# Optimization experiments

Measured on AMD Instinct MI355X. Metric: run time of the kernel, lower is better.

The kernel has to match this reference:

```python
import jax, jax.numpy as jnp
import numpy as np

B, NUM_OBJECTS, NUM_ATTRS, T = 8, 128, 4, 12
MAX_CONCEPTS, EMBED_DIM, IDENTITY_DIM, ATTENTION_DIM, HIDDEN_DIM = 2048, 128, 64, 64, 256
OP_MODE, OP_INSERT, OP_TRANSFER = 0, 1, 2


def setup_inputs() -> dict:
    key = jax.random.key(0)
    ks = jax.random.split(key, 24)
    def rn(k, shape, s=0.05):
        return s * jax.random.normal(k, shape, dtype=jnp.float32)
    return {
        'scene': jax.random.randint(ks[0], (B, NUM_OBJECTS, NUM_ATTRS), 0, MAX_CONCEPTS - 1),
        'program_op': jax.random.randint(ks[1], (B, T), 0, 3),
        'program_arg': jax.random.randint(ks[2], (B, T), 0, MAX_CONCEPTS),
        'attr_emb_in': rn(ks[3], (MAX_CONCEPTS, EMBED_DIM)),
        'attr_emb_out': rn(ks[4], (MAX_CONCEPTS, EMBED_DIM)),
        'attr_emb_id': rn(ks[5], (MAX_CONCEPTS, IDENTITY_DIM)),
        'concept_emb_in': rn(ks[6], (MAX_CONCEPTS, EMBED_DIM)),
        'concept_emb_out': rn(ks[7], (MAX_CONCEPTS, EMBED_DIM)),
        'concept_emb_id': rn(ks[8], (MAX_CONCEPTS, IDENTITY_DIM)),
        'embed_init': rn(ks[9], (EMBED_DIM,)),
        'identity_init': rn(ks[10], (IDENTITY_DIM,)),
        'attention_init': jnp.zeros((ATTENTION_DIM,), dtype=jnp.float32),
        'axon_w1': rn(ks[11], (HIDDEN_DIM, ATTENTION_DIM + IDENTITY_DIM)),
        'axon_b1': rn(ks[12], (HIDDEN_DIM,)),
        'axon_w2': rn(ks[13], (ATTENTION_DIM, HIDDEN_DIM)),
        'axon_b2': rn(ks[14], (ATTENTION_DIM,)),
        'meta_w1': rn(ks[15], (HIDDEN_DIM, EMBED_DIM + ATTENTION_DIM)),
        'meta_b1': rn(ks[16], (HIDDEN_DIM,)),
        'meta_w2': rn(ks[17], (ATTENTION_DIM, HIDDEN_DIM)),
        'meta_b2': rn(ks[18], (ATTENTION_DIM,)),
    }


def _mlp(x, w1, b1, w2, b2):
    # torch Linear convention: y = x @ W.T + b
    return jnp.maximum(x @ w1.T + b1, 0.0) @ w2.T + b2


def reference(scene, program_op, program_arg, attr_emb_in, attr_emb_out, attr_emb_id,
              concept_emb_in, concept_emb_out, concept_emb_id,
              embed_init, identity_init, attention_init,
              axon_w1, axon_b1, axon_w2, axon_b2,
              meta_w1, meta_b1, meta_w2, meta_b2):
    Bq, N, _ = scene.shape
    C = MAX_CONCEPTS + N  # dim_concept
    mask = (scene != -1).astype(jnp.float32)  # (B,N,A) non-background mask
    def embed_bg(E):
        return (E[scene + 1] * mask[..., None]).sum(2)  # (B,N,D)
    objects_in = embed_bg(attr_emb_in)
    objects_out = embed_bg(attr_emb_out)
    objects_id = embed_bg(attr_emb_id)

    rep = lambda w: jnp.broadcast_to(w[None], (Bq,) + w.shape)
    dendron = jnp.concatenate([rep(concept_emb_in), objects_in], 1)    # (B,C,E)
    axon = jnp.concatenate([rep(concept_emb_out), objects_out], 1)     # (B,C,E)
    identity = jnp.concatenate([rep(concept_emb_id), objects_id], 1)   # (B,C,Id)
    weight_matrix = jnp.einsum('bie,bje->bij', dendron, axon)           # (B,C,C)

    arguments = concept_emb_out[program_arg]                            # (B,T,E)
    is_mode = (program_op == OP_MODE).astype(jnp.float32)               # (B,T)
    is_insert = (program_op == OP_INSERT).astype(jnp.float32)
    is_transfer = (program_op == OP_TRANSFER).astype(jnp.float32)

    meta0 = jnp.broadcast_to(attention_init[None], (Bq, ATTENTION_DIM))
    att0 = jnp.broadcast_to(attention_init[None, None], (Bq, C, ATTENTION_DIM))

    def step(carry, xs):
        meta, attention = carry
        arg_i, m, ins, tr = xs  # (B,E), (B,), (B,), (B,)
        new_meta = _mlp(jnp.concatenate([meta, arg_i], 1), meta_w1, meta_b1, meta_w2, meta_b2)
        meta = m[:, None] * new_meta + (1.0 - m[:, None]) * meta
        # (arguments * axon).mean over embed dim -> (B,C)
        proj = jnp.einsum('be,bce->bc', arg_i, axon) / EMBED_DIM
        attention_insert = meta[:, None, :] * proj[:, :, None]          # (B,C,A)
        attended_weight = weight_matrix * attention.mean(2)[:, None, :] # (B,C,C)
        ia = jnp.concatenate([identity, attention], 2)                  # (B,C,Id+A)
        # (attended_weight[:,:,:,None] * ia[:,None]).mean(2) == matmul / C
        gathered = jnp.einsum('bij,bjd->bid', attended_weight, ia) / C  # (B,C,Id+A)
        attention_transfer = _mlp(gathered, axon_w1, axon_b1, axon_w2, axon_b2) + gathered[..., IDENTITY_DIM:]
        attention = attention + ins[:, None, None] * attention_insert + tr[:, None, None] * attention_transfer
        attention = jnp.clip(jnp.where(attention >= 0, attention, 0.01 * attention), -1.0, 2.0)
        return (meta, attention), (attention, attention_insert, attention_transfer)

    xs = (jnp.swapaxes(arguments, 0, 1), is_mode.T, is_insert.T, is_transfer.T)
    (meta, attention), (att_hist, ins_hist, trans_hist) = jax.lax.scan(step, (meta0, att0), xs)
    output_softmax = jax.nn.log_softmax(attention.mean(2), axis=1)  # (B,C)
    return (output_softmax, att_hist, ins_hist, trans_hist)
```

## Files before the change

kernel.cpp:

```cpp
#include <hip/hip_runtime.h>

#define B 8
#define NOBJ 128
#define NATTR 4
#define T 12
#define MC 2048
#define E 128
#define IDD 64
#define AD 64
#define HD 256
#define C 2176

typedef short s16x8 __attribute__((ext_vector_type(8)));
typedef float f32x4 __attribute__((ext_vector_type(4)));

__device__ inline unsigned short f2b(float f) {
  union { float f; unsigned u; } v; v.f = f;
  unsigned r = v.u + 0x7FFFu + ((v.u >> 16) & 1u);
  return (unsigned short)(r >> 16);
}
__device__ inline float b2f(unsigned short u) {
  union { unsigned u; float f; } v; v.u = ((unsigned)u) << 16;
  return v.f;
}

__device__ __forceinline__ void st_coh_u64(unsigned long long* p, unsigned long long v) {
  __hip_atomic_store(p, v, __ATOMIC_RELAXED, __HIP_MEMORY_SCOPE_AGENT);
}
__device__ __forceinline__ unsigned long long ld_coh_u64(const unsigned long long* p) {
  return __hip_atomic_load(p, __ATOMIC_RELAXED, __HIP_MEMORY_SCOPE_AGENT);
}
__device__ __forceinline__ void st_coh_u32(unsigned* p, unsigned v) {
  __hip_atomic_store(p, v, __ATOMIC_RELAXED, __HIP_MEMORY_SCOPE_AGENT);
}
__device__ __forceinline__ unsigned ld_coh_u32(const unsigned* p) {
  return __hip_atomic_load(p, __ATOMIC_RELAXED, __HIP_MEMORY_SCOPE_AGENT);
}

__device__ __forceinline__ int gidx(int r, int c) {
  return r * 128 + ((((c >> 3) ^ (r & 15)) << 3) | (c & 7));
}
__device__ __forceinline__ int hidx(int r, int c) {
  return r * 256 + ((((c >> 3) ^ (r & 15)) << 3) | (c & 7));
}
__device__ __forceinline__ int mtidx(int r, int c) {
  return r * 128 + ((((c >> 3) ^ (r & 15)) << 3) | (c & 7));
}

__global__ __launch_bounds__(256) void k_setup1(
    const int* __restrict__ scene,
    const float* __restrict__ aein, const float* __restrict__ aeout,
    const float* __restrict__ aeid,
    const float* __restrict__ cein, const float* __restrict__ ceout,
    const float* __restrict__ ceid,
    const float* __restrict__ aw1, const float* __restrict__ aw2,
    const float* __restrict__ mw1, const float* __restrict__ mw2,
    unsigned short* __restrict__ dendron_bf, float* __restrict__ axon,
    float* __restrict__ identity,
    unsigned short* __restrict__ w1_bf, unsigned short* __restrict__ w2_bf,
    float* __restrict__ mw1T, float* __restrict__ mw2T,
    unsigned* __restrict__ mflag) {
  int blk = blockIdx.x;
  int tid = threadIdx.x;
  if (blk < 4352) {
    int gid = blk * 2 + (tid >> 7);
    int e = tid & 127;
    int b = gid / C, j = gid % C;
    float din, dout, did = 0.f;
    if (j < MC) {
      din  = cein[j * E + e];
      dout = ceout[j * E + e];
      if (e < IDD) did = ceid[j * IDD + e];
    } else {
      int obj = j - MC;
      float sIn = 0.f, sOut = 0.f, sId = 0.f;
      for (int a = 0; a < NATTR; a++) {
        int s = scene[(b * NOBJ + obj) * NATTR + a];
        float m = (s != -1) ? 1.f : 0.f;
        int idx = s + 1;
        sIn  += aein[idx * E + e] * m;
        sOut += aeout[idx * E + e] * m;
        if (e < IDD) sId += aeid[idx * IDD + e] * m;
      }
      din = sIn; dout = sOut; did = sId;
    }
    dendron_bf[(size_t)gid * E + e] = f2b(din);
    axon[(size_t)gid * E + e] = dout;
    if (e < IDD) identity[(size_t)gid * IDD + e] = did;
  } else if (blk < 4544) {
    int i = (blk - 4352) * 256 + tid;
    if (i < HD * E)  w1_bf[i] = f2b(aw1[i]);
    if (i < AD * HD) w2_bf[i] = f2b(aw2[i]);
    if (i < 192 * HD) { int c = i / HD, k = i % HD; mw1T[c * HD + k] = mw1[k * 192 + c]; }
    if (i < HD * AD)  { int k = i / AD, a = i % AD; mw2T[k * AD + a] = mw2[a * HD + k]; }
  } else {
    if (tid < B * 16) mflag[tid] = 0u;
  }
}

__global__ __launch_bounds__(256) void k_setup2(
    const float* __restrict__ axon, const float* __restrict__ identity,
    const float* __restrict__ att_init,
    const int* __restrict__ prog_op, const int* __restrict__ prog_arg,
    const float* __restrict__ ceout,
    const float* __restrict__ mw1T, const float* __restrict__ mb1,
    const float* __restrict__ mw2T, const float* __restrict__ mb2,
    unsigned short* __restrict__ axonT, unsigned short* __restrict__ idT_g,
    unsigned short* __restrict__ siaT, float* __restrict__ att_g,
    float* __restrict__ meta_all, float* __restrict__ proj_all) {
  int blk = blockIdx.x;
  int tid = threadIdx.x;
  if (blk < 272) {
    int b = blk / 34, jc = blk % 34;
    int j0 = jc * 64;
    __shared__ float ax[64][129];
    __shared__ float idb[64][65];
    int lane = tid & 63, lr = lane & 15;
    float s = att_init[lane];
    s += __shfl_xor(s, 1, 64);  s += __shfl_xor(s, 2, 64);
    s += __shfl_xor(s, 4, 64);  s += __shfl_xor(s, 8, 64);
    s += __shfl_xor(s, 16, 64); s += __shfl_xor(s, 32, 64);
    float am0 = s * (1.f / AD);
    for (int i = tid; i < 64 * 128; i += 256) {
      int j = i >> 7, e = i & 127;
      ax[j][e] = axon[(size_t)(b * C + j0 + j) * E + e];
    }
    for (int i = tid; i < 64 * 64; i += 256) {
      int j = i >> 6, d = i & 63;
      idb[j][d] = identity[(size_t)(b * C + j0 + j) * IDD + d];
    }
    __syncthreads();
    for (int i = tid; i < 128 * 64; i += 256) {
      int e = i >> 6, jj = i & 63;
      axonT[(size_t)(b * E + e) * C + j0 + jj] = f2b(ax[jj][e]);
    }
    for (int i = tid; i < 64 * 64; i += 256) {
      int d = i >> 6, jj = i & 63;
      idT_g[(size_t)(b * 64 + d) * C + j0 + jj] = f2b(idb[jj][d]);
      siaT[(size_t)(b * 128 + d) * C + j0 + jj] = f2b(idb[jj][d] * am0);
      siaT[(size_t)(b * 128 + 64 + d) * C + j0 + jj] = f2b(att_init[d] * am0);
    }
    {
      float* ag = att_g + (size_t)blk * 4096 + tid * 16;
      #pragma unroll
      for (int n = 0; n < 4; n++) {
        float v0 = att_init[n * 16 + lr];
        #pragma unroll
        for (int v = 0; v < 4; v++) ag[n * 4 + v] = v0;
      }
    }
  } else if (blk < 280) {
    int b = blk - 272;
    __shared__ float x[192];
    __shared__ float h[HD];
    __shared__ float meta[AD];
    if (tid < AD) meta[tid] = att_init[tid];
    __syncthreads();
    for (int t = 0; t < T; t++) {
      int arg = prog_arg[b * T + t];
      if (tid < AD) x[tid] = meta[tid];
      else if (tid < 192) x[tid] = ceout[arg * E + (tid - 64)];
      __syncthreads();
      float s = mb1[tid];
      for (int c = 0; c < 192; c++) s += x[c] * mw1T[c * HD + tid];
      h[tid] = fmaxf(s, 0.f);
      __syncthreads();
      if (tid < AD) {
        float o = mb2[tid];
        for (int k = 0; k < HD; k++) o += h[k] * mw2T[k * AD + tid];
        float m = (prog_op[b * T + t] == 0) ? 1.f : 0.f;
        float nm = m * o + (1.f - m) * meta[tid];
        meta[tid] = nm;
        meta_all[(t * B + b) * AD + tid] = nm;
      }
      __syncthreads();
    }
  } else {
    int gid = (blk - 280) * 4 + (tid >> 6);
    int lane = tid & 63;
    int b = gid / C, i = gid % C;
    float a0 = axon[(size_t)gid * E + lane];
    float a1 = axon[(size_t)gid * E + 64 + lane];
    for (int t = 0; t < T; t++) {
      int arg = prog_arg[b * T + t];
      float p = a0 * ceout[arg * E + lane] + a1 * ceout[arg * E + 64 + lane];
      for (int off = 1; off < 64; off <<= 1) p += __shfl_xor(p, off, 64);
      if (lane == 0) proj_all[(size_t)(t * B + b) * C + i] = p * (1.f / E);
    }
  }
}

__global__ __launch_bounds__(256) void k_step(
    int t,
    const unsigned short* __restrict__ dendron_bf,
    const unsigned short* __restrict__ axonT,
    const unsigned short* __restrict__ idT_g,
    const unsigned short* __restrict__ siaT_in,
    const unsigned short* __restrict__ w1_bf, const float* __restrict__ b1g,
    const unsigned short* __restrict__ w2_bf, const float* __restrict__ b2g,
    const float* __restrict__ proj_all, const float* __restrict__ meta_all,
    const int* __restrict__ prog_op,
    unsigned long long* __restrict__ Mt64,
    float* __restrict__ att_g, unsigned short* __restrict__ siaT_out,
    float* __restrict__ rowmean,
    float* __restrict__ att_hist, float* __restrict__ ins_hist,
    float* __restrict__ trans_hist,
    unsigned* __restrict__ mflag) {
  const int blk = blockIdx.x;
  const int b = blk / 34, ch = blk % 34, j0 = ch * 64;
  const int tid = threadIdx.x;
  const int w = tid >> 6, lane = tid & 63, lr = lane & 15, lg = lane >> 4;

  __shared__ unsigned short smem[24576];
  __shared__ float am_l[64];
  unsigned short* g_l = smem;
  unsigned short* mt  = smem + 8192;
  unsigned short* h_l = smem + 8192;
  float* mred = (float*)smem;

  const f32x4 z = {0.f, 0.f, 0.f, 0.f};
  const unsigned ph = (unsigned)(t + 1);

  float att[4][4];
  {
    const f32x4* ag = (const f32x4*)(att_g + (size_t)blk * 4096 + tid * 16);
    #pragma unroll
    for (int n = 0; n < 4; n++) {
      f32x4 v4 = ag[n];
      #pragma unroll
      for (int v = 0; v < 4; v++) att[n][v] = v4[v];
    }
  }

  if (ch < 16) {
    int d0 = (ch >> 2) * 32, e0 = (ch & 3) * 32;
    const unsigned short* ap0 = siaT_in + (size_t)(b * 128 + d0 + lr) * C + w * 544 + lg * 8;
    const unsigned short* ap1 = ap0 + (size_t)16 * C;
    const unsigned short* bp0 = axonT + (size_t)(b * E + e0 + lr) * C + w * 544 + lg * 8;
    const unsigned short* bp1 = bp0 + (size_t)16 * C;
    f32x4 a00 = z, a01 = z, a10 = z, a11 = z;
    #pragma unroll 4
    for (int kk = 0; kk < 17; kk++) {
      int k0 = kk * 32;
      s16x8 A0 = *(const s16x8*)(ap0 + k0);
      s16x8 A1 = *(const s16x8*)(ap1 + k0);
      s16x8 B0 = *(const s16x8*)(bp0 + k0);
      s16x8 B1 = *(const s16x8*)(bp1 + k0);
      a00 = __builtin_amdgcn_mfma_f32_16x16x32_bf16(A0, B0, a00, 0, 0, 0);
      a01 = __builtin_amdgcn_mfma_f32_16x16x32_bf16(A0, B1, a01, 0, 0, 0);
      a10 = __builtin_amdgcn_mfma_f32_16x16x32_bf16(A1, B0, a10, 0, 0, 0);
      a11 = __builtin_amdgcn_mfma_f32_16x16x32_bf16(A1, B1, a11, 0, 0, 0);
    }
    #pragma unroll
    for (int v = 0; v < 4; v++) {
      mred[(w * 32 + lg * 4 + v) * 33 + lr]          = a00[v];
      mred[(w * 32 + lg * 4 + v) * 33 + 16 + lr]     = a01[v];
      mred[(w * 32 + 16 + lg * 4 + v) * 33 + lr]     = a10[v];
      mred[(w * 32 + 16 + lg * 4 + v) * 33 + 16 + lr] = a11[v];
    }
    __syncthreads();
    {
      int r = tid >> 3, c = (tid & 7) * 4;
      float s0 = 0.f, s1 = 0.f, s2 = 0.f, s3 = 0.f;
      #pragma unroll
      for (int w4 = 0; w4 < 4; w4++) {
        const float* p = &mred[(w4 * 32 + r) * 33 + c];
        s0 += p[0]; s1 += p[1]; s2 += p[2]; s3 += p[3];
      }
      unsigned long long pk = (unsigned long long)f2b(s0)
                            | ((unsigned long long)f2b(s1) << 16)
                            | ((unsigned long long)f2b(s2) << 32)
                            | ((unsigned long long)f2b(s3) << 48);
      st_coh_u64(Mt64 + (((size_t)(b * 128 + d0 + r) * 128) + e0 + c) / 4, pk);
    }
    asm volatile("s_waitcnt vmcnt(0)" ::: "memory");
    __syncthreads();
    if (tid == 0) st_coh_u32(mflag + b * 16 + ch, ph);
  }
  if (tid < 16) {
    while (ld_coh_u32(mflag + b * 16 + tid) < ph) __builtin_amdgcn_s_sleep(1);
  }
  __syncthreads();
  {
    const unsigned long long* mtp = Mt64 + (size_t)b * 4096;
    #pragma unroll
    for (int k = 0; k < 16; k++) {
      int idx = tid + k * 256;
      unsigned long long v = ld_coh_u64(mtp + idx);
      int r = idx >> 5, c4 = (idx & 31) * 4;
      *(unsigned long long*)&mt[mtidx(r, c4)] = v;
    }
  }
  __syncthreads();
  {
    s16x8 afr[4];
    #pragma unroll
    for (int ke = 0; ke < 4; ke++)
      afr[ke] = *(const s16x8*)(dendron_bf + (size_t)(b * C + j0 + w * 16 + lr) * E + ke * 32 + lg * 8);
    #pragma unroll
    for (int n = 0; n < 8; n++) {
      f32x4 acc = z;
      #pragma unroll
      for (int ke = 0; ke < 4; ke++) {
        s16x8 bf = *(const s16x8*)&mt[mtidx(n * 16 + lr, ke * 32 + lg * 8)];
        acc = __builtin_amdgcn_mfma_f32_16x16x32_bf16(afr[ke], bf, acc, 0, 0, 0);
      }
      #pragma unroll
      for (int v = 0; v < 4; v++)
        g_l[gidx(w * 16 + lg * 4 + v, n * 16 + lr)] = f2b(acc[v] * (1.f / C));
    }
  }
  __syncthreads();
  {
    s16x8 gf[4];
    #pragma unroll
    for (int kd = 0; kd < 4; kd++)
      gf[kd] = *(const s16x8*)&g_l[gidx(w * 16 + lr, kd * 32 + lg * 8)];
    #pragma unroll
    for (int n = 0; n < 16; n++) {
      f32x4 acc = z;
      #pragma unroll
      for (int kd = 0; kd < 4; kd++) {
        s16x8 bf = *(const s16x8*)(w1_bf + (size_t)(n * 16 + lr) * E + kd * 32 + lg * 8);
        acc = __builtin_amdgcn_mfma_f32_16x16x32_bf16(gf[kd], bf, acc, 0, 0, 0);
      }
      float b1v = b1g[n * 16 + lr];
      #pragma unroll
      for (int v = 0; v < 4; v++)
        h_l[hidx(w * 16 + lg * 4 + v, n * 16 + lr)] = f2b(fmaxf(acc[v] + b1v, 0.f));
    }
  }
  __syncthreads();
  {
    s16x8 hf[8];
    #pragma unroll
    for (int kk = 0; kk < 8; kk++)
      hf[kk] = *(const s16x8*)&h_l[hidx(w * 16 + lr, kk * 32 + lg * 8)];
    int op = prog_op[b * T + t];
    float insF = (op == 1) ? 1.f : 0.f, trF = (op == 2) ? 1.f : 0.f;
    float projv[4];
    #pragma unroll
    for (int v = 0; v < 4; v++)
      projv[v] = proj_all[(size_t)(t * B + b) * C + j0 + w * 16 + lg * 4 + v];
    #pragma unroll
    for (int n = 0; n < 4; n++) {
      f32x4 acc = z;
      #pragma unroll
      for (int kk = 0; kk < 8; kk++) {
        s16x8 bf = *(const s16x8*)(w2_bf + (size_t)(n * 16 + lr) * HD + kk * 32 + lg * 8);
        acc = __builtin_amdgcn_mfma_f32_16x16x32_bf16(hf[kk], bf, acc, 0, 0, 0);
      }
      int a = n * 16 + lr;
      float b2v = b2g[a];
      float meta_a = meta_all[(size_t)(t * B + b) * AD + a];
      #pragma unroll
      for (int v = 0; v < 4; v++) {
        int row = lg * 4 + v;
        int i = j0 + w * 16 + row;
        float transfer = acc[v] + b2v + b2f(g_l[gidx(w * 16 + row, 64 + a)]);
        float insert = meta_a * projv[v];
        float attv = att[n][v] + insF * insert + trF * transfer;
        attv = (attv >= 0.f) ? attv : 0.01f * attv;
        attv = fminf(fmaxf(attv, -1.f), 2.f);
        att[n][v] = attv;
        size_t hi = (((size_t)t * B + b) * C + i) * AD + a;
        __builtin_nontemporal_store(attv, att_hist + hi);
        __builtin_nontemporal_store(insert, ins_hist + hi);
        __builtin_nontemporal_store(transfer, trans_hist + hi);
      }
    }
  }
  float amr[4];
  {
    float s[4];
    #pragma unroll
    for (int v = 0; v < 4; v++) s[v] = att[0][v] + att[1][v] + att[2][v] + att[3][v];
    #pragma unroll
    for (int v = 0; v < 4; v++) {
      s[v] += __shfl_xor(s[v], 1, 64);
      s[v] += __shfl_xor(s[v], 2, 64);
      s[v] += __shfl_xor(s[v], 4, 64);
      s[v] += __shfl_xor(s[v], 8, 64);
      amr[v] = s[v] * (1.f / AD);
    }
    if (lr == 0) {
      #pragma unroll
      for (int v = 0; v < 4; v++) {
        am_l[w * 16 + lg * 4 + v] = amr[v];
        rowmean[(size_t)b * C + j0 + w * 16 + lg * 4 + v] = amr[v];
      }
    }
  }
  {
    f32x4* ag = (f32x4*)(att_g + (size_t)blk * 4096 + tid * 16);
    #pragma unroll
    for (int n = 0; n < 4; n++) {
      f32x4 v4;
      #pragma unroll
      for (int v = 0; v < 4; v++) v4[v] = att[n][v];
      ag[n] = v4;
      unsigned long long pk = 0;
      #pragma unroll
      for (int v = 0; v < 4; v++)
        pk |= (unsigned long long)f2b(att[n][v] * amr[v]) << (16 * v);
      *(unsigned long long*)(siaT_out + (size_t)(b * 128 + 64 + n * 16 + lr) * C + j0 + w * 16 + lg * 4) = pk;
    }
  }
  __syncthreads();
  #pragma unroll
  for (int k = 0; k < 2; k++) {
    int idx = tid + k * 256;
    int d = idx >> 3, part = idx & 7;
    int j = part * 8;
    s16x8 iv = *(const s16x8*)(idT_g + (size_t)(b * 64 + d) * C + j0 + j);
    s16x8 ov;
    #pragma unroll
    for (int m = 0; m < 8; m++)
      ov[m] = (short)f2b(b2f((unsigned short)iv[m]) * am_l[j + m]);
    *(s16x8*)(siaT_out + (size_t)(b * 128 + d) * C + j0 + j) = ov;
  }
}

__global__ void k_softmax(const float* __restrict__ rowmean, float* __restrict__ out) {
  int b = blockIdx.x;
  __shared__ float am[C];
  __shared__ float red[256];
  int tid = threadIdx.x;
  for (int i = tid; i < C; i += 256) am[i] = rowmean[(size_t)b * C + i];
  __syncthreads();
  float mx = -1e30f;
  for (int i = tid; i < C; i += 256) mx = fmaxf(mx, am[i]);
  red[tid] = mx; __syncthreads();
  for (int s = 128; s > 0; s >>= 1) { if (tid < s) red[tid] = fmaxf(red[tid], red[tid + s]); __syncthreads(); }
  mx = red[0]; __syncthreads();
  float sm = 0.f;
  for (int i = tid; i < C; i += 256) sm += expf(am[i] - mx);
  red[tid] = sm; __syncthreads();
  for (int s = 128; s > 0; s >>= 1) { if (tid < s) red[tid] += red[tid + s]; __syncthreads(); }
  float lse = logf(red[0]) + mx;
  for (int i = tid; i < C; i += 256) out[(size_t)b * C + i] = am[i] - lse;
}

extern "C" void kernel_launch(void* const* d_in, const int* in_sizes, int n_in,
                              void* d_out, int out_size, void* d_ws, size_t ws_size,
                              hipStream_t stream) {
  const int* scene     = (const int*)d_in[0];
  const int* prog_op   = (const int*)d_in[1];
  const int* prog_arg  = (const int*)d_in[2];
  const float* aein    = (const float*)d_in[3];
  const float* aeout   = (const float*)d_in[4];
  const float* aeid    = (const float*)d_in[5];
  const float* cein    = (const float*)d_in[6];
  const float* ceout   = (const float*)d_in[7];
  const float* ceid    = (const float*)d_in[8];
  const float* att_init = (const float*)d_in[11];
  const float* aw1 = (const float*)d_in[12];
  const float* ab1 = (const float*)d_in[13];
  const float* aw2 = (const float*)d_in[14];
  const float* ab2 = (const float*)d_in[15];
  const float* mw1 = (const float*)d_in[16];
  const float* mb1 = (const float*)d_in[17];
  const float* mw2 = (const float*)d_in[18];
  const float* mb2 = (const float*)d_in[19];

  char* ws = (char*)d_ws;
  size_t off = 0;
  auto carve = [&](size_t bytes) { char* p = ws + off; off += (bytes + 255) & ~(size_t)255; return p; };
  float* axon      = (float*)carve((size_t)B * C * E * 4);
  float* identity  = (float*)carve((size_t)B * C * IDD * 4);
  float* proj_all  = (float*)carve((size_t)T * B * C * 4);
  float* meta_all  = (float*)carve((size_t)T * B * AD * 4);
  float* mw1T      = (float*)carve((size_t)192 * HD * 4);
  float* mw2T      = (float*)carve((size_t)HD * AD * 4);
  float* rowmean   = (float*)carve((size_t)B * C * 4);
  float* att_g     = (float*)carve((size_t)272 * 4096 * 4);
  unsigned short* dendron_bf = (unsigned short*)carve((size_t)B * C * E * 2);
  unsigned short* axonT      = (unsigned short*)carve((size_t)B * E * C * 2);
  unsigned short* idT_g      = (unsigned short*)carve((size_t)B * 64 * C * 2);
  unsigned short* siaT       = (unsigned short*)carve((size_t)B * 128 * C * 2);
  unsigned long long* Mt64   = (unsigned long long*)carve((size_t)B * 4096 * 8);
  unsigned short* w1_bf      = (unsigned short*)carve((size_t)HD * E * 2);
  unsigned short* w2_bf      = (unsigned short*)carve((size_t)AD * HD * 2);
  unsigned*       mflag      = (unsigned*)carve(1024);

  float* out_sm     = (float*)d_out;
  float* att_hist   = out_sm + B * C;
  float* ins_hist   = att_hist + (size_t)T * B * C * AD;
  float* trans_hist = ins_hist + (size_t)T * B * C * AD;

  k_setup1<<<dim3(4545), dim3(256), 0, stream>>>(scene, aein, aeout, aeid, cein, ceout, ceid,
                                                 aw1, aw2, mw1, mw2,
                                                 dendron_bf, axon, identity,
                                                 w1_bf, w2_bf, mw1T, mw2T, mflag);
  k_setup2<<<dim3(1368), dim3(256), 0, stream>>>(axon, identity, att_init,
                                                 prog_op, prog_arg, ceout,
                                                 mw1T, mb1, mw2T, mb2,
                                                 axonT, idT_g, siaT, att_g,
                                                 meta_all, proj_all);
  for (int t = 0; t < T; t++) {
    k_step<<<dim3(272), dim3(256), 0, stream>>>(t, dendron_bf, axonT, idT_g, siaT,
                                                w1_bf, ab1, w2_bf, ab2,
                                                proj_all, meta_all, prog_op,
                                                Mt64, att_g, siaT, rowmean,
                                                att_hist, ins_hist, trans_hist, mflag);
  }
  k_softmax<<<dim3(B), dim3(256), 0, stream>>>(rowmean, out_sm);
}
```

Before: 655.4 us.

## Fuse all timesteps and softmax into one persistent kernel with flag-based sync

```diff
diff --git a/kernel.cpp b/kernel.cpp
--- a/kernel.cpp
+++ b/kernel.cpp
@@ -35,6 +35,21 @@
 }
 __device__ __forceinline__ unsigned ld_coh_u32(const unsigned* p) {
   return __hip_atomic_load(p, __ATOMIC_RELAXED, __HIP_MEMORY_SCOPE_AGENT);
+}
+__device__ __forceinline__ void st_coh_f32(float* p, float v) {
+  union { float f; unsigned u; } c; c.f = v;
+  __hip_atomic_store((unsigned*)p, c.u, __ATOMIC_RELAXED, __HIP_MEMORY_SCOPE_AGENT);
+}
+__device__ __forceinline__ float ld_coh_f32(const float* p) {
+  union { unsigned u; float f; } c;
+  c.u = __hip_atomic_load((const unsigned*)p, __ATOMIC_RELAXED, __HIP_MEMORY_SCOPE_AGENT);
+  return c.f;
+}
+__device__ __forceinline__ s16x8 ld_coh_b16x8(const unsigned short* p) {
+  union { unsigned long long u[2]; s16x8 v; } r;
+  r.u[0] = ld_coh_u64((const unsigned long long*)p);
+  r.u[1] = ld_coh_u64((const unsigned long long*)p + 1);
+  return r.v;
 }
 
 __device__ __forceinline__ int gidx(int r, int c) {
@@ -59,7 +74,7 @@
     float* __restrict__ identity,
     unsigned short* __restrict__ w1_bf, unsigned short* __restrict__ w2_bf,
     float* __restrict__ mw1T, float* __restrict__ mw2T,
-    unsigned* __restrict__ mflag) {
+    unsigned* __restrict__ flags) {
   int blk = blockIdx.x;
   int tid = threadIdx.x;
   if (blk < 4352) {
@@ -94,7 +109,7 @@
     if (i < 192 * HD) { int c = i / HD, k = i % HD; mw1T[c * HD + k] = mw1[k * 192 + c]; }
     if (i < HD * AD)  { int k = i / AD, a = i % AD; mw2T[k * AD + a] = mw2[a * HD + k]; }
   } else {
-    if (tid < B * 16) mflag[tid] = 0u;
+    for (int i = tid; i < 576; i += 256) flags[i] = 0u;
   }
 }
 
@@ -106,7 +121,7 @@
     const float* __restrict__ mw1T, const float* __restrict__ mb1,
     const float* __restrict__ mw2T, const float* __restrict__ mb2,
     unsigned short* __restrict__ axonT, unsigned short* __restrict__ idT_g,
-    unsigned short* __restrict__ siaT, float* __restrict__ att_g,
+    unsigned short* __restrict__ siaT,
     float* __restrict__ meta_all, float* __restrict__ proj_all) {
   int blk = blockIdx.x;
   int tid = threadIdx.x;
@@ -115,7 +130,7 @@
     int j0 = jc * 64;
     __shared__ float ax[64][129];
     __shared__ float idb[64][65];
-    int lane = tid & 63, lr = lane & 15;
+    int lane = tid & 63;
     float s = att_init[lane];
     s += __shfl_xor(s, 1, 64);  s += __shfl_xor(s, 2, 64);
     s += __shfl_xor(s, 4, 64);  s += __shfl_xor(s, 8, 64);
@@ -139,15 +154,6 @@
       idT_g[(size_t)(b * 64 + d) * C + j0 + jj] = f2b(idb[jj][d]);
       siaT[(size_t)(b * 128 + d) * C + j0 + jj] = f2b(idb[jj][d] * am0);
       siaT[(size_t)(b * 128 + 64 + d) * C + j0 + jj] = f2b(att_init[d] * am0);
-    }
-    {
-      float* ag = att_g + (size_t)blk * 4096 + tid * 16;
-      #pragma unroll
-      for (int n = 0; n < 4; n++) {
-        float v0 = att_init[n * 16 + lr];
-        #pragma unroll
-        for (int v = 0; v < 4; v++) ag[n * 4 + v] = v0;
-      }
     }
   } else if (blk < 280) {
     int b = blk - 272;
@@ -190,22 +196,21 @@
   }
 }
 
-__global__ __launch_bounds__(256) void k_step(
-    int t,
+__global__ __launch_bounds__(256, 2) void k_steps(
     const unsigned short* __restrict__ dendron_bf,
     const unsigned short* __restrict__ axonT,
     const unsigned short* __restrict__ idT_g,
-    const unsigned short* __restrict__ siaT_in,
+    unsigned short* __restrict__ siaT,
     const unsigned short* __restrict__ w1_bf, const float* __restrict__ b1g,
     const unsigned short* __restrict__ w2_bf, const float* __restrict__ b2g,
     const float* __restrict__ proj_all, const float* __restrict__ meta_all,
-    const int* __restrict__ prog_op,
+    const int* __restrict__ prog_op, const float* __restrict__ att_init,
     unsigned long long* __restrict__ Mt64,
-    float* __restrict__ att_g, unsigned short* __restrict__ siaT_out,
-    float* __restrict__ rowmean,
+    float* __restrict__ rowmean, float* __restrict__ out,
     float* __restrict__ att_hist, float* __restrict__ ins_hist,
     float* __restrict__ trans_hist,
-    unsigned* __restrict__ mflag) {
+    unsigned* __restrict__ mflag, unsigned* __restrict__ cflag,
+    unsigned* __restrict__ sflag) {
   const int blk = blockIdx.x;
   const int b = blk / 34, ch = blk % 34, j0 = ch * 64;
   const int tid = threadIdx.x;
@@ -213,232 +218,250 @@
 
   __shared__ unsigned short smem[24576];
   __shared__ float am_l[64];
+  __shared__ float red[256];
   unsigned short* g_l = smem;
   unsigned short* mt  = smem + 8192;
   unsigned short* h_l = smem + 8192;
-  float* mred = (float*)smem;
 
   const f32x4 z = {0.f, 0.f, 0.f, 0.f};
-  const unsigned ph = (unsigned)(t + 1);
 
   float att[4][4];
-  {
-    const f32x4* ag = (const f32x4*)(att_g + (size_t)blk * 4096 + tid * 16);
+  #pragma unroll
+  for (int n = 0; n < 4; n++) {
+    float v0 = att_init[n * 16 + lr];
     #pragma unroll
-    for (int n = 0; n < 4; n++) {
-      f32x4 v4 = ag[n];
-      #pragma unroll
-      for (int v = 0; v < 4; v++) att[n][v] = v4[v];
-    }
+    for (int v = 0; v < 4; v++) att[n][v] = v0;
   }
-
-  if (ch < 16) {
-    int d0 = (ch >> 2) * 32, e0 = (ch & 3) * 32;
-    const unsigned short* ap0 = siaT_in + (size_t)(b * 128 + d0 + lr) * C + w * 544 + lg * 8;
-    const unsigned short* ap1 = ap0 + (size_t)16 * C;
-    const unsigned short* bp0 = axonT + (size_t)(b * E + e0 + lr) * C + w * 544 + lg * 8;
-    const unsigned short* bp1 = bp0 + (size_t)16 * C;
-    f32x4 a00 = z, a01 = z, a10 = z, a11 = z;
-    #pragma unroll 4
-    for (int kk = 0; kk < 17; kk++) {
-      int k0 = kk * 32;
-      s16x8 A0 = *(const s16x8*)(ap0 + k0);
-      s16x8 A1 = *(const s16x8*)(ap1 + k0);
-      s16x8 B0 = *(const s16x8*)(bp0 + k0);
-      s16x8 B1 = *(const s16x8*)(bp1 + k0);
-      a00 = __builtin_amdgcn_mfma_f32_16x16x32_bf16(A0, B0, a00, 0, 0, 0);
-      a01 = __builtin_amdgcn_mfma_f32_16x16x32_bf16(A0, B1, a01, 0, 0, 0);
-      a10 = __builtin_amdgcn_mfma_f32_16x16x32_bf16(A1, B0, a10, 0, 0, 0);
-      a11 = __builtin_amdgcn_mfma_f32_16x16x32_bf16(A1, B1, a11, 0, 0, 0);
-    }
-    #pragma unroll
-    for (int v = 0; v < 4; v++) {
-      mred[(w * 32 + lg * 4 + v) * 33 + lr]          = a00[v];
-      mred[(w * 32 + lg * 4 + v) * 33 + 16 + lr]     = a01[v];
-      mred[(w * 32 + 16 + lg * 4 + v) * 33 + lr]     = a10[v];
-      mred[(w * 32 + 16 + lg * 4 + v) * 33 + 16 + lr] = a11[v];
+  s16x8 afr[4];
+  #pragma unroll
+  for (int ke = 0; ke < 4; ke++)
+    afr[ke] = *(const s16x8*)(dendron_bf + (size_t)(b * C + j0 + w * 16 + lr) * E + ke * 32 + lg * 8);
+
+  float amr[4];
+
+  for (int t = 0; t < T; t++) {
+    const unsigned ph = (unsigned)(t + 1);
+    if (ch < 4) {
+      if (t > 0) {
+        if (tid < 34) {
+          while (ld_coh_u32(cflag + b * 34 + tid) < (unsigned)t) __builtin_amdgcn_s_sleep(2);
+        }
+      }
+      __syncthreads();
+      const int d0 = ch * 32;
+      const int eh = w & 1, kh = w >> 1;
+      const int kbase = kh * 1088;
+      const unsigned short* ap0 = siaT + (size_t)(b * 128 + d0 + lr) * C + kbase + lg * 8;
+      const unsigned short* ap1 = ap0 + (size_t)16 * C;
+      const unsigned short* bp  = axonT + (size_t)(b * E + eh * 64 + lr) * C + kbase + lg * 8;
+      f32x4 pa[2][4];
+      #pragma unroll
+      for (int dp = 0; dp < 2; dp++)
+        #pragma unroll
+        for (int n = 0; n < 4; n++) pa[dp][n] = z;
+      for (int kk = 0; kk < 34; kk++) {
+        int k0 = kk * 32;
+        s16x8 A0 = ld_coh_b16x8(ap0 + k0);
+        s16x8 A1 = ld_coh_b16x8(ap1 + k0);
+        #pragma unroll
+        for (int n = 0; n < 4; n++) {
+          s16x8 Bn = *(const s16x8*)(bp + (size_t)n * 16 * C + k0);
+          pa[0][n] = __builtin_amdgcn_mfma_f32_16x16x32_bf16(A0, Bn, pa[0][n], 0, 0, 0);
+          pa[1][n] = __builtin_amdgcn_mfma_f32_16x16x32_bf16(A1, Bn, pa[1][n], 0, 0, 0);
+        }
+      }
+      float* pls = (float*)smem;
+      #pragma unroll
+      for (int dp = 0; dp < 2; dp++)
+        #pragma unroll
+        for (int n = 0; n < 4; n++)
+          #pragma unroll
+          for (int v = 0; v < 4; v++)
+            pls[(kh * 32 + dp * 16 + lg * 4 + v) * 132 + eh * 64 + n * 16 + lr] = pa[dp][n][v];
+      __syncthreads();
+      {
+        int r = tid >> 3, cb = (tid & 7) * 16;
+        const float* p0 = pls + r * 132 + cb;
+        const float* p1 = pls + (32 + r) * 132 + cb;
+        #pragma unroll
+        for (int q = 0; q < 4; q++) {
+          unsigned long long pk = 0;
+          #pragma unroll
+          for (int x = 0; x < 4; x++) {
+            float sv = p0[q * 4 + x] + p1[q * 4 + x];
+            pk |= (unsigned long long)f2b(sv) << (16 * x);
+          }
+          st_coh_u64(Mt64 + ((size_t)(b * 128 + d0 + r) * 128 + cb + q * 4) / 4, pk);
+        }
+      }
+      asm volatile("s_waitcnt vmcnt(0)" ::: "memory");
+      __syncthreads();
+      if (tid == 0) st_coh_u32(mflag + b * 4 + ch, ph);
+    }
+    if (tid < 4) {
+      while (ld_coh_u32(mflag + b * 4 + tid) < ph) __builtin_amdgcn_s_sleep(2);
     }
     __syncthreads();
     {
-      int r = tid >> 3, c = (tid & 7) * 4;
-      float s0 = 0.f, s1 = 0.f, s2 = 0.f, s3 = 0.f;
-      #pragma unroll
-      for (int w4 = 0; w4 < 4; w4++) {
-        const float* p = &mred[(w4 * 32 + r) * 33 + c];
-        s0 += p[0]; s1 += p[1]; s2 += p[2]; s3 += p[3];
-      }
-      unsigned long long pk = (unsigned long long)f2b(s0)
-                            | ((unsigned long long)f2b(s1) << 16)
-                            | ((unsigned long long)f2b(s2) << 32)
-                            | ((unsigned long long)f2b(s3) << 48);
-      st_coh_u64(Mt64 + (((size_t)(b * 128 + d0 + r) * 128) + e0 + c) / 4, pk);
-    }
-    asm volatile("s_waitcnt vmcnt(0)" ::: "memory");
-    __syncthreads();
-    if (tid == 0) st_coh_u32(mflag + b * 16 + ch, ph);
+      const unsigned long long* mtp = Mt64 + (size_t)b * 4096;
+      #pragma unroll
+      for (int k = 0; k < 16; k++) {
+        int idx = tid + k * 256;
+        unsigned long long v = ld_coh_u64(mtp + idx);
+        int r = idx >> 5, c4 = (idx & 31) * 4;
+        *(unsigned long long*)&mt[mtidx(r, c4)] = v;
+      }
+    }
+    __syncthreads();
+    {
+      #pragma unroll
+      for (int n = 0; n < 8; n++) {
+        f32x4 acc = z;
+        #pragma unroll
+        for (int ke = 0; ke < 4; ke++) {
+          s16x8 bf = *(const s16x8*)&mt[mtidx(n * 16 + lr, ke * 32 + lg * 8)];
+          acc = __builtin_amdgcn_mfma_f32_16x16x32_bf16(afr[ke], bf, acc, 0, 0, 0);
+        }
+        #pragma unroll
+        for (int v = 0; v < 4; v++)
+          g_l[gidx(w * 16 + lg * 4 + v, n * 16 + lr)] = f2b(acc[v] * (1.f / C));
+      }
+    }
+    __syncthreads();
+    {
+      s16x8 gf[4];
+      #pragma unroll
+      for (int kd = 0; kd < 4; kd++)
+        gf[kd] = *(const s16x8*)&g_l[gidx(w * 16 + lr, kd * 32 + lg * 8)];
+      #pragma unroll
+      for (int n = 0; n < 16; n++) {
+        f32x4 acc = z;
+        #pragma unroll
+        for (int kd = 0; kd < 4; kd++) {
+          s16x8 bf = *(const s16x8*)(w1_bf + (size_t)(n * 16 + lr) * E + kd * 32 + lg * 8);
+          acc = __builtin_amdgcn_mfma_f32_16x16x32_bf16(gf[kd], bf, acc, 0, 0, 0);
+        }
+        float b1v = b1g[n * 16 + lr];
+        #pragma unroll
+        for (int v = 0; v < 4; v++)
+          h_l[hidx(w * 16 + lg * 4 + v, n * 16 + lr)] = f2b(fmaxf(acc[v] + b1v, 0.f));
+      }
+    }
+    __syncthreads();
+    {
+      s16x8 hf[8];
+      #pragma unroll
+      for (int kk = 0; kk < 8; kk++)
+        hf[kk] = *(const s16x8*)&h_l[hidx(w * 16 + lr, kk * 32 + lg * 8)];
+      int op = prog_op[b * T + t];
+      float insF = (op == 1) ? 1.f : 0.f, trF = (op == 2) ? 1.f : 0.f;
+      float projv[4];
+      #pragma unroll
+      for (int v = 0; v < 4; v++)
+        projv[v] = proj_all[(size_t)(t * B + b) * C + j0 + w * 16 + lg * 4 + v];
+      #pragma unroll
+      for (int n = 0; n < 4; n++) {
+        f32x4 acc = z;
+        #pragma unroll
+        for (int kk = 0; kk < 8; kk++) {
+          s16x8 bf = *(const s16x8*)(w2_bf + (size_t)(n * 16 + lr) * HD + kk * 32 + lg * 8);
+          acc = __builtin_amdgcn_mfma_f32_16x16x32_bf16(hf[kk], bf, acc, 0, 0, 0);
+        }
+        int a = n * 16 + lr;
+        float b2v = b2g[a];
+        float meta_a = meta_all[(size_t)(t * B + b) * AD + a];
+        #pragma unroll
+        for (int v = 0; v < 4; v++) {
+          int row = lg * 4 + v;
+          int i = j0 + w * 16 + row;
+          float transfer = acc[v] + b2v + b2f(g_l[gidx(w * 16 + row, 64 + a)]);
+          float insert = meta_a * projv[v];
+          float attv = att[n][v] + insF * insert + trF * transfer;
+          attv = (attv >= 0.f) ? attv : 0.01f * attv;
+          attv = fminf(fmaxf(attv, -1.f), 2.f);
+          att[n][v] = attv;
+          size_t hi = (((size_t)t * B + b) * C + i) * AD + a;
+          __builtin_nontemporal_store(attv, att_hist + hi);
+          __builtin_nontemporal_store(insert, ins_hist + hi);
+          __builtin_nontemporal_store(transfer, trans_hist + hi);
+        }
+      }
+    }
+    {
+      float s[4];
+      #pragma unroll
+      for (int v = 0; v < 4; v++) s[v] = att[0][v] + att[1][v] + att[2][v] + att[3][v];
+      #pragma unroll
+      for (int v = 0; v < 4; v++) {
+        s[v] += __shfl_xor(s[v], 1, 64);
+        s[v] += __shfl_xor(s[v], 2, 64);
+        s[v] += __shfl_xor(s[v], 4, 64);
+        s[v] += __shfl_xor(s[v], 8, 64);
+        amr[v] = s[v] * (1.f / AD);
+      }
+      if (lr == 0) {
+        #pragma unroll
+        for (int v = 0; v < 4; v++) am_l[w * 16 + lg * 4 + v] = amr[v];
+      }
+    }
+    if (t < T - 1) {
+      #pragma unroll
+      for (int n = 0; n < 4; n++) {
+        unsigned long long pk = 0;
+        #pragma unroll
+        for (int v = 0; v < 4; v++)
+          pk |= (unsigned long long)f2b(att[n][v] * amr[v]) << (16 * v);
+        st_coh_u64((unsigned long long*)(siaT + (size_t)(b * 128 + 64 + n * 16 + lr) * C + j0 + w * 16 + lg * 4), pk);
+      }
+      __syncthreads();
+      #pragma unroll
+      for (int k2 = 0; k2 < 2; k2++) {
+        int idx = tid + k2 * 256;
+        int d = idx >> 3, part = idx & 7;
+        int j = part * 8;
+        s16x8 iv = *(const s16x8*)(idT_g + (size_t)(b * 64 + d) * C + j0 + j);
+        union { s16x8 v; unsigned long long u[2]; } ov;
+        #pragma unroll
+        for (int m = 0; m < 8; m++)
+          ov.v[m] = (short)f2b(b2f((unsigned short)iv[m]) * am_l[j + m]);
+        unsigned long long* dst = (unsigned long long*)(siaT + (size_t)(b * 128 + d) * C + j0 + j);
+        st_coh_u64(dst, ov.u[0]);
+        st_coh_u64(dst + 1, ov.u[1]);
+      }
+      asm volatile("s_waitcnt vmcnt(0)" ::: "memory");
+      __syncthreads();
+      if (tid == 0) st_coh_u32(cflag + b * 34 + ch, ph);
+      __syncthreads();
+    }
   }
-  if (tid < 16) {
-    while (ld_coh_u32(mflag + b * 16 + tid) < ph) __builtin_amdgcn_s_sleep(1);
-  }
-  __syncthreads();
-  {
-    const unsigned long long* mtp = Mt64 + (size_t)b * 4096;
-    #pragma unroll
-    for (int k = 0; k < 16; k++) {
-      int idx = tid + k * 256;
-      unsigned long long v = ld_coh_u64(mtp + idx);
-      int r = idx >> 5, c4 = (idx & 31) * 4;
-      *(unsigned long long*)&mt[mtidx(r, c4)] = v;
-    }
-  }
-  __syncthreads();
-  {
-    s16x8 afr[4];
-    #pragma unroll
-    for (int ke = 0; ke < 4; ke++)
-      afr[ke] = *(const s16x8*)(dendron_bf + (size_t)(b * C + j0 + w * 16 + lr) * E + ke * 32 + lg * 8);
-    #pragma unroll
-    for (int n = 0; n < 8; n++) {
-      f32x4 acc = z;
-      #pragma unroll
-      for (int ke = 0; ke < 4; ke++) {
-        s16x8 bf = *(const s16x8*)&mt[mtidx(n * 16 + lr, ke * 32 + lg * 8)];
-        acc = __builtin_amdgcn_mfma_f32_16x16x32_bf16(afr[ke], bf, acc, 0, 0, 0);
-      }
-      #pragma unroll
-      for (int v = 0; v < 4; v++)
-        g_l[gidx(w * 16 + lg * 4 + v, n * 16 + lr)] = f2b(acc[v] * (1.f / C));
-    }
-  }
-  __syncthreads();
-  {
-    s16x8 gf[4];
-    #pragma unroll
-    for (int kd = 0; kd < 4; kd++)
-      gf[kd] = *(const s16x8*)&g_l[gidx(w * 16 + lr, kd * 32 + lg * 8)];
-    #pragma unroll
-    for (int n = 0; n < 16; n++) {
-      f32x4 acc = z;
-      #pragma unroll
-      for (int kd = 0; kd < 4; kd++) {
-        s16x8 bf = *(const s16x8*)(w1_bf + (size_t)(n * 16 + lr) * E + kd * 32 + lg * 8);
-        acc = __builtin_amdgcn_mfma_f32_16x16x32_bf16(gf[kd], bf, acc, 0, 0, 0);
-      }
-      float b1v = b1g[n * 16 + lr];
-      #pragma unroll
-      for (int v = 0; v < 4; v++)
-        h_l[hidx(w * 16 + lg * 4 + v, n * 16 + lr)] = f2b(fmaxf(acc[v] + b1v, 0.f));
-    }
-  }
-  __syncthreads();
-  {
-    s16x8 hf[8];
-    #pragma unroll
-    for (int kk = 0; kk < 8; kk++)
-      hf[kk] = *(const s16x8*)&h_l[hidx(w * 16 + lr, kk * 32 + lg * 8)];
-    int op = prog_op[b * T + t];
-    float insF = (op == 1) ? 1.f : 0.f, trF = (op == 2) ? 1.f : 0.f;
-    float projv[4];
+  if (lr == 0) {
     #pragma unroll
     for (int v = 0; v < 4; v++)
-      projv[v] = proj_all[(size_t)(t * B + b) * C + j0 + w * 16 + lg * 4 + v];
-    #pragma unroll
-    for (int n = 0; n < 4; n++) {
-      f32x4 acc = z;
-      #pragma unroll
-      for (int kk = 0; kk < 8; kk++) {
-        s16x8 bf = *(const s16x8*)(w2_bf + (size_t)(n * 16 + lr) * HD + kk * 32 + lg * 8);
-        acc = __builtin_amdgcn_mfma_f32_16x16x32_bf16(hf[kk], bf, acc, 0, 0, 0);
-      }
-      int a = n * 16 + lr;
-      float b2v = b2g[a];
-      float meta_a = meta_all[(size_t)(t * B + b) * AD + a];
-      #pragma unroll
-      for (int v = 0; v < 4; v++) {
-        int row = lg * 4 + v;
-        int i = j0 + w * 16 + row;
-        float transfer = acc[v] + b2v + b2f(g_l[gidx(w * 16 + row, 64 + a)]);
-        float insert = meta_a * projv[v];
-        float attv = att[n][v] + insF * insert + trF * transfer;
-        attv = (attv >= 0.f) ? attv : 0.01f * attv;
-        attv = fminf(fmaxf(attv, -1.f), 2.f);
-        att[n][v] = attv;
-        size_t hi = (((size_t)t * B + b) * C + i) * AD + a;
-        __builtin_nontemporal_store(attv, att_hist + hi);
-        __builtin_nontemporal_store(insert, ins_hist + hi);
-        __builtin_nontemporal_store(transfer, trans_hist + hi);
-      }
-    }
+      st_coh_f32(rowmean + (size_t)b * C + j0 + w * 16 + lg * 4 + v, amr[v]);
   }
-  float amr[4];
-  {
-    float s[4];
-    #pragma unroll
-    for (int v = 0; v < 4; v++) s[v] = att[0][v] + att[1][v] + att[2][v] + att[3][v];
-    #pragma unroll
-    for (int v = 0; v < 4; v++) {
-      s[v] += __shfl_xor(s[v], 1, 64);
-      s[v] += __shfl_xor(s[v], 2, 64);
-      s[v] += __shfl_xor(s[v], 4, 64);
-      s[v] += __shfl_xor(s[v], 8, 64);
-      amr[v] = s[v] * (1.f / AD);
-    }
-    if (lr == 0) {
-      #pragma unroll
-      for (int v = 0; v < 4; v++) {
-        am_l[w * 16 + lg * 4 + v] = amr[v];
-        rowmean[(size_t)b * C + j0 + w * 16 + lg * 4 + v] = amr[v];
-      }
-    }
+  asm volatile("s_waitcnt vmcnt(0)" ::: "memory");
+  __syncthreads();
+  if (tid == 0) st_coh_u32(sflag + b * 34 + ch, 1u);
+  if (ch == 0) {
+    if (tid < 34) {
+      while (ld_coh_u32(sflag + b * 34 + tid) < 1u) __builtin_amdgcn_s_sleep(2);
+    }
+    __syncthreads();
+    float* am = (float*)smem;
+    for (int i = tid; i < C; i += 256) am[i] = ld_coh_f32(rowmean + (size_t)b * C + i);
+    __syncthreads();
+    float mx = -1e30f;
+    for (int i = tid; i < C; i += 256) mx = fmaxf(mx, am[i]);
+    red[tid] = mx; __syncthreads();
+    for (int s2 = 128; s2 > 0; s2 >>= 1) { if (tid < s2) red[tid] = fmaxf(red[tid], red[tid + s2]); __syncthreads(); }
+    mx = red[0]; __syncthreads();
+    float sm = 0.f;
+    for (int i = tid; i < C; i += 256) sm += expf(am[i] - mx);
+    red[tid] = sm; __syncthreads();
+    for (int s2 = 128; s2 > 0; s2 >>= 1) { if (tid < s2) red[tid] += red[tid + s2]; __syncthreads(); }
+    float lse = logf(red[0]) + mx;
+    for (int i = tid; i < C; i += 256) out[(size_t)b * C + i] = am[i] - lse;
   }
-  {
-    f32x4* ag = (f32x4*)(att_g + (size_t)blk * 4096 + tid * 16);
-    #pragma unroll
-    for (int n = 0; n < 4; n++) {
-      f32x4 v4;
-      #pragma unroll
-      for (int v = 0; v < 4; v++) v4[v] = att[n][v];
-      ag[n] = v4;
-      unsigned long long pk = 0;
-      #pragma unroll
-      for (int v = 0; v < 4; v++)
-        pk |= (unsigned long long)f2b(att[n][v] * amr[v]) << (16 * v);
-      *(unsigned long long*)(siaT_out + (size_t)(b * 128 + 64 + n * 16 + lr) * C + j0 + w * 16 + lg * 4) = pk;
-    }
-  }
-  __syncthreads();
-  #pragma unroll
-  for (int k = 0; k < 2; k++) {
-    int idx = tid + k * 256;
-    int d = idx >> 3, part = idx & 7;
-    int j = part * 8;
-    s16x8 iv = *(const s16x8*)(idT_g + (size_t)(b * 64 + d) * C + j0 + j);
-    s16x8 ov;
-    #pragma unroll
-    for (int m = 0; m < 8; m++)
-      ov[m] = (short)f2b(b2f((unsigned short)iv[m]) * am_l[j + m]);
-    *(s16x8*)(siaT_out + (size_t)(b * 128 + d) * C + j0 + j) = ov;
-  }
-}
-
-__global__ void k_softmax(const float* __restrict__ rowmean, float* __restrict__ out) {
-  int b = blockIdx.x;
-  __shared__ float am[C];
-  __shared__ float red[256];
-  int tid = threadIdx.x;
-  for (int i = tid; i < C; i += 256) am[i] = rowmean[(size_t)b * C + i];
-  __syncthreads();
-  float mx = -1e30f;
-  for (int i = tid; i < C; i += 256) mx = fmaxf(mx, am[i]);
-  red[tid] = mx; __syncthreads();
-  for (int s = 128; s > 0; s >>= 1) { if (tid < s) red[tid] = fmaxf(red[tid], red[tid + s]); __syncthreads(); }
-  mx = red[0]; __syncthreads();
-  float sm = 0.f;
-  for (int i = tid; i < C; i += 256) sm += expf(am[i] - mx);
-  red[tid] = sm; __syncthreads();
-  for (int s = 128; s > 0; s >>= 1) { if (tid < s) red[tid] += red[tid + s]; __syncthreads(); }
-  float lse = logf(red[0]) + mx;
-  for (int i = tid; i < C; i += 256) out[(size_t)b * C + i] = am[i] - lse;
 }
 
 extern "C" void kernel_launch(void* const* d_in, const int* in_sizes, int n_in,
@@ -473,7 +496,6 @@
   float* mw1T      = (float*)carve((size_t)192 * HD * 4);
   float* mw2T      = (float*)carve((size_t)HD * AD * 4);
   float* rowmean   = (float*)carve((size_t)B * C * 4);
-  float* att_g     = (float*)carve((size_t)272 * 4096 * 4);
   unsigned short* dendron_bf = (unsigned short*)carve((size_t)B * C * E * 2);
   unsigned short* axonT      = (unsigned short*)carve((size_t)B * E * C * 2);
   unsigned short* idT_g      = (unsigned short*)carve((size_t)B * 64 * C * 2);
@@ -481,7 +503,10 @@
   unsigned long long* Mt64   = (unsigned long long*)carve((size_t)B * 4096 * 8);
   unsigned short* w1_bf      = (unsigned short*)carve((size_t)HD * E * 2);
   unsigned short* w2_bf      = (unsigned short*)carve((size_t)AD * HD * 2);
-  unsigned*       mflag      = (unsigned*)carve(1024);
+  unsigned*       flags      = (unsigned*)carve(4096);
+  unsigned*       mflag = flags;
+  unsigned*       cflag = flags + 32;
+  unsigned*       sflag = flags + 304;
 
   float* out_sm     = (float*)d_out;
   float* att_hist   = out_sm + B * C;
@@ -491,18 +516,16 @@
   k_setup1<<<dim3(4545), dim3(256), 0, stream>>>(scene, aein, aeout, aeid, cein, ceout, ceid,
                                                  aw1, aw2, mw1, mw2,
                                                  dendron_bf, axon, identity,
-                                                 w1_bf, w2_bf, mw1T, mw2T, mflag);
+                                                 w1_bf, w2_bf, mw1T, mw2T, flags);
   k_setup2<<<dim3(1368), dim3(256), 0, stream>>>(axon, identity, att_init,
                                                  prog_op, prog_arg, ceout,
                                                  mw1T, mb1, mw2T, mb2,
-                                                 axonT, idT_g, siaT, att_g,
+                                                 axonT, idT_g, siaT,
                                                  meta_all, proj_all);
-  for (int t = 0; t < T; t++) {
-    k_step<<<dim3(272), dim3(256), 0, stream>>>(t, dendron_bf, axonT, idT_g, siaT,
-                                                w1_bf, ab1, w2_bf, ab2,
-                                                proj_all, meta_all, prog_op,
-                                                Mt64, att_g, siaT, rowmean,
-                                                att_hist, ins_hist, trans_hist, mflag);
-  }
-  k_softmax<<<dim3(B), dim3(256), 0, stream>>>(rowmean, out_sm);
-}
+  k_steps<<<dim3(272), dim3(256), 0, stream>>>(dendron_bf, axonT, idT_g, siaT,
+                                               w1_bf, ab1, w2_bf, ab2,
+                                               proj_all, meta_all, prog_op, att_init,
+                                               Mt64, rowmean, out_sm,
+                                               att_hist, ins_hist, trans_hist,
+                                               mflag, cflag, sflag);
+}
```

New measurement: 1.580 ms. 141% more time.
